# Performance work log

Measured on AMD Instinct MI355X. Metric: run time of the kernel, lower is better.

## Reference

```python
import jax, jax.numpy as jnp
import numpy as np

NEG_SLOPE = 0.2  # PyG GATConv default negative_slope


def setup_inputs() -> dict:
    key = jax.random.key(0)
    k_x, k_e, k_w, k_as, k_ad = jax.random.split(key, 5)
    B, F, N, D, E, L = 2, 16, 5000, 128, 40000, 3
    x = jax.random.normal(k_x, (B, F, N, D), dtype=jnp.float32)
    edge_index = jax.random.randint(k_e, (B, F, 2, E), 0, N, dtype=jnp.int64)
    Ws = jax.random.normal(k_w, (L, D, D), dtype=jnp.float32) / np.float32(np.sqrt(D))
    att_src = jax.random.normal(k_as, (L, D), dtype=jnp.float32) / np.float32(np.sqrt(D))
    att_dst = jax.random.normal(k_ad, (L, D), dtype=jnp.float32) / np.float32(np.sqrt(D))
    bias = jnp.zeros((L, D), dtype=jnp.float32)
    return {"x": x, "edge_index": edge_index, "Ws": Ws,
            "att_src": att_src, "att_dst": att_dst, "bias": bias}


def _gat_layer(h, src, dst, n, W, a_s, a_d, b):
    # h: [n, D] node features; src/dst: [E_tot] edge endpoints (self-loops included)
    h2 = h @ W                                   # [n, D] transformed features
    s = h2 @ a_s                                 # [n] per-node source score
    d = h2 @ a_d                                 # [n] per-node dest score
    e = jax.nn.leaky_relu(s[src] + d[dst], NEG_SLOPE)   # [E_tot] raw attention
    m = jax.lax.stop_gradient(jax.ops.segment_max(e, dst, num_segments=n))
    ex = jnp.exp(e - m[dst])                     # numerically stable softmax per dst
    denom = jax.ops.segment_sum(ex, dst, num_segments=n)
    alpha = ex / denom[dst]                      # [E_tot] normalized attention
    out = jax.ops.segment_sum(alpha[:, None] * h2[src], dst, num_segments=n) + b
    return jax.nn.relu(out)


def reference(x, edge_index, Ws, att_src, att_dst, bias):
    B, F, N, D = x.shape
    n = B * F * N
    h = x.reshape(n, D)
    # faithful to torch: (BF,2,E).view(2,-1) is a raw row-major reshape
    ei = edge_index.reshape(2, -1)
    loop = jnp.arange(n, dtype=ei.dtype)         # PyG GATConv adds self-loops
    src = jnp.concatenate([ei[0], loop])
    dst = jnp.concatenate([ei[1], loop])
    for l in range(Ws.shape[0]):                 # fixed small layer loop
        h = _gat_layer(h, src, dst, n, Ws[l], att_src[l], att_dst[l], bias[l])
    return h.reshape(B, F, N, D)
```

## Files before the change

### kernel.cpp

```cpp
#include <hip/hip_runtime.h>
#include <math.h>

#define NODES_TOTAL 160000
#define NODES_REAL  5000
#define D 128
#define NEG 0.2f
#define KP 136
#define HL (128 * KP)
#define WT_L (2 * HL)

typedef unsigned short ushort_t;
typedef unsigned int uint_t;
typedef __attribute__((ext_vector_type(8))) __bf16 bf16x8;
typedef __attribute__((ext_vector_type(4))) float f32x4;
union BF8 { bf16x8 v; ushort_t u[8]; };

__device__ __forceinline__ void split2(float x, ushort_t& hi, ushort_t& lo) {
    unsigned u = __float_as_uint(x);
    hi = (ushort_t)(u >> 16);
    float hif = __uint_as_float(u & 0xffff0000u);
    lo = (ushort_t)(__float_as_uint(x - hif) >> 16);
}
__device__ __forceinline__ uint_t encmax(float f) {
    uint_t b = __float_as_uint(f);
    return b ^ ((uint_t)((int)b >> 31) | 0x80000000u);
}
__device__ __forceinline__ float decmax(uint_t u) {
    uint_t b = (u & 0x80000000u) ? (u ^ 0x80000000u) : ~u;
    return __uint_as_float(b);
}

__global__ void zero_kernel(int* counts, uint_t* gmaxu) {
    int i = blockIdx.x * blockDim.x + threadIdx.x;
    if (i < NODES_REAL) counts[i] = 0;
    if (i < 3) gmaxu[i] = 0u;
}

__global__ void rank_kernel(const int* __restrict__ ei, int* __restrict__ counts,
                            ushort_t* __restrict__ rank16, int Eh) {
    int e = blockIdx.x * blockDim.x + threadIdx.x;
    if (e < Eh) {
        int d = ei[Eh + e];
        int r = atomicAdd(&counts[d], 1);
        rank16[e] = (ushort_t)r;
    }
}

__global__ void scan_kernel(const int* __restrict__ counts, int* __restrict__ offs) {
    __shared__ int sd[1024];
    int t = threadIdx.x;
    int pre[5]; int sum = 0;
    #pragma unroll
    for (int u = 0; u < 5; ++u) {
        int idx = t * 5 + u;
        int c = (idx < NODES_REAL) ? counts[idx] : 0;
        pre[u] = sum; sum += c;
    }
    sd[t] = sum;
    __syncthreads();
    int run = sum;
    for (int o = 1; o < 1024; o <<= 1) {
        int v = (t >= o) ? sd[t - o] : 0;
        __syncthreads();
        sd[t] += v;
        __syncthreads();
    }
    int excl = sd[t] - run;
    #pragma unroll
    for (int u = 0; u < 5; ++u) {
        int idx = t * 5 + u;
        if (idx < NODES_REAL) offs[idx] = excl + pre[u];
    }
    if (t == 1023) offs[NODES_REAL] = excl + run;
}

__global__ void scatter_det(const int* __restrict__ ei, const int* __restrict__ offs,
                            const ushort_t* __restrict__ rank16, ushort_t* __restrict__ esrc,
                            int Eh) {
    int e = blockIdx.x * blockDim.x + threadIdx.x;
    if (e < Eh) {
        int s = ei[e];
        int d = ei[Eh + e];
        esrc[offs[d] + (int)rank16[e]] = (ushort_t)s;
    }
}

__global__ void wsplit_kernel(const float* __restrict__ Ws, ushort_t* __restrict__ Wt) {
    int l  = blockIdx.x >> 3;
    int n  = (blockIdx.x & 7) * 16 + (threadIdx.x >> 4);
    int k0 = (threadIdx.x & 15) * 8;
    const float* src = Ws + (size_t)l * D * D;
    union { ushort_t u[8]; uint4 v; } hi, lo;
    #pragma unroll
    for (int j = 0; j < 8; ++j) split2(src[(size_t)(k0 + j) * D + n], hi.u[j], lo.u[j]);
    ushort_t* dhi = Wt + (size_t)l * WT_L + n * KP + k0;
    *(uint4*)dhi = hi.v;
    *(uint4*)(dhi + HL) = lo.v;
}

__global__ __launch_bounds__(256)
void mlp3_kernel(const float* __restrict__ x, const ushort_t* __restrict__ Wt,
                 const float* __restrict__ bs, float* __restrict__ out) {
    __shared__ ushort_t Wl[WT_L];
    __shared__ float scr[4][2][16][132];
    int tid = threadIdx.x;
    int w = tid >> 6, lane = tid & 63, q = lane >> 4, m16 = lane & 15;
    int row0 = NODES_REAL + blockIdx.x * 128 + w * 32;

    float4 xa[2][4][2];
    #pragma unroll
    for (int rt = 0; rt < 2; ++rt) {
        int r = row0 + rt * 16 + m16;
        if (r > NODES_TOTAL - 1) r = NODES_TOTAL - 1;
        #pragma unroll
        for (int kc = 0; kc < 4; ++kc) {
            const float* gp = x + (size_t)r * D + kc * 32 + q * 8;
            xa[rt][kc][0] = *(const float4*)gp;
            xa[rt][kc][1] = *(const float4*)(gp + 4);
        }
    }

    f32x4 acc[2][8];
    #pragma unroll
    for (int l = 0; l < 3; ++l) {
        __syncthreads();
        {
            const uint4* gw = (const uint4*)(Wt + (size_t)l * WT_L);
            uint4* lw = (uint4*)Wl;
            #pragma unroll
            for (int r = 0; r < 17; ++r) lw[r * 256 + tid] = gw[r * 256 + tid];
        }
        __syncthreads();

        #pragma unroll
        for (int rt = 0; rt < 2; ++rt)
            #pragma unroll
            for (int ct = 0; ct < 8; ++ct) acc[rt][ct] = (f32x4){0.f, 0.f, 0.f, 0.f};

        #pragma unroll
        for (int kc = 0; kc < 4; ++kc) {
            BF8 ahi[2], alo[2];
            #pragma unroll
            for (int rt = 0; rt < 2; ++rt) {
                float xv[8];
                if (l == 0) {
                    float4 v0 = xa[rt][kc][0], v1 = xa[rt][kc][1];
                    xv[0]=v0.x; xv[1]=v0.y; xv[2]=v0.z; xv[3]=v0.w;
                    xv[4]=v1.x; xv[5]=v1.y; xv[6]=v1.z; xv[7]=v1.w;
                } else {
                    const float* sp = &scr[w][rt][m16][kc * 32 + q * 8];
                    float4 v0 = *(const float4*)sp, v1 = *(const float4*)(sp + 4);
                    xv[0]=v0.x; xv[1]=v0.y; xv[2]=v0.z; xv[3]=v0.w;
                    xv[4]=v1.x; xv[5]=v1.y; xv[6]=v1.z; xv[7]=v1.w;
                }
                #pragma unroll
                for (int j = 0; j < 8; ++j) split2(xv[j], ahi[rt].u[j], alo[rt].u[j]);
            }
            #pragma unroll
            for (int ct = 0; ct < 8; ++ct) {
                const ushort_t* bp = Wl + (ct * 16 + m16) * KP + kc * 32 + q * 8;
                bf16x8 bhi = *(const bf16x8*)bp;
                bf16x8 blo = *(const bf16x8*)(bp + HL);
                #pragma unroll
                for (int rt = 0; rt < 2; ++rt) {
                    acc[rt][ct] = __builtin_amdgcn_mfma_f32_16x16x32_bf16(ahi[rt].v, bhi, acc[rt][ct], 0, 0, 0);
                    acc[rt][ct] = __builtin_amdgcn_mfma_f32_16x16x32_bf16(ahi[rt].v, blo, acc[rt][ct], 0, 0, 0);
                    acc[rt][ct] = __builtin_amdgcn_mfma_f32_16x16x32_bf16(alo[rt].v, bhi, acc[rt][ct], 0, 0, 0);
                }
            }
        }
        float bv[8];
        #pragma unroll
        for (int ct = 0; ct < 8; ++ct) bv[ct] = bs[l * D + ct * 16 + m16];
        #pragma unroll
        for (int rt = 0; rt < 2; ++rt)
            #pragma unroll
            for (int ct = 0; ct < 8; ++ct)
                #pragma unroll
                for (int reg = 0; reg < 4; ++reg)
                    scr[w][rt][q * 4 + reg][ct * 16 + m16] =
                        fmaxf(acc[rt][ct][reg] + bv[ct], 0.f);
    }
    #pragma unroll
    for (int i = 0; i < 16; ++i) {
        int rowl = i * 2 + (lane >> 5);
        int rt = rowl >> 4, r16 = rowl & 15;
        int grow = row0 + rowl;
        float4 v = *(const float4*)&scr[w][rt][r16][(lane & 31) * 4];
        if (grow < NODES_TOTAL)
            *(float4*)&out[(size_t)grow * D + (lane & 31) * 4] = v;
    }
}

__global__ __launch_bounds__(256)
void gsmall_kernel(const float* __restrict__ hin, const ushort_t* __restrict__ Wlg,
                   const float* __restrict__ a_s, const float* __restrict__ a_d,
                   float* __restrict__ h2, float* __restrict__ sv, float* __restrict__ dv,
                   uint_t* __restrict__ gmaxu) {
    __shared__ ushort_t Wl[WT_L];
    int tid = threadIdx.x;
    {
        const uint4* gw = (const uint4*)Wlg;
        uint4* lw = (uint4*)Wl;
        #pragma unroll
        for (int r = 0; r < 17; ++r) lw[r * 256 + tid] = gw[r * 256 + tid];
    }
    int w = tid >> 6, lane = tid & 63, q = lane >> 4, m16 = lane & 15;
    int row0 = blockIdx.x * 128 + w * 32;
    f32x4 acc[2][8];
    #pragma unroll
    for (int rt = 0; rt < 2; ++rt)
        #pragma unroll
        for (int ct = 0; ct < 8; ++ct) acc[rt][ct] = (f32x4){0.f, 0.f, 0.f, 0.f};
    float4 xa[2][4][2];
    #pragma unroll
    for (int rt = 0; rt < 2; ++rt) {
        int r = row0 + rt * 16 + m16;
        if (r > NODES_REAL - 1) r = NODES_REAL - 1;
        #pragma unroll
        for (int kc = 0; kc < 4; ++kc) {
            const float* gp = hin + (size_t)r * D + kc * 32 + q * 8;
            xa[rt][kc][0] = *(const float4*)gp;
            xa[rt][kc][1] = *(const float4*)(gp + 4);
        }
    }
    __syncthreads();
    #pragma unroll
    for (int kc = 0; kc < 4; ++kc) {
        BF8 ahi[2], alo[2];
        #pragma unroll
        for (int rt = 0; rt < 2; ++rt) {
            float4 v0 = xa[rt][kc][0], v1 = xa[rt][kc][1];
            float xv[8] = {v0.x, v0.y, v0.z, v0.w, v1.x, v1.y, v1.z, v1.w};
            #pragma unroll
            for (int j = 0; j < 8; ++j) split2(xv[j], ahi[rt].u[j], alo[rt].u[j]);
        }
        #pragma unroll
        for (int ct = 0; ct < 8; ++ct) {
            const ushort_t* bp = Wl + (ct * 16 + m16) * KP + kc * 32 + q * 8;
            bf16x8 bhi = *(const bf16x8*)bp;
            bf16x8 blo = *(const bf16x8*)(bp + HL);
            #pragma unroll
            for (int rt = 0; rt < 2; ++rt) {
                acc[rt][ct] = __builtin_amdgcn_mfma_f32_16x16x32_bf16(ahi[rt].v, bhi, acc[rt][ct], 0, 0, 0);
                acc[rt][ct] = __builtin_amdgcn_mfma_f32_16x16x32_bf16(ahi[rt].v, blo, acc[rt][ct], 0, 0, 0);
                acc[rt][ct] = __builtin_amdgcn_mfma_f32_16x16x32_bf16(alo[rt].v, bhi, acc[rt][ct], 0, 0, 0);
            }
        }
    }
    #pragma unroll
    for (int rt = 0; rt < 2; ++rt)
        #pragma unroll
        for (int reg = 0; reg < 4; ++reg) {
            int grow = row0 + rt * 16 + q * 4 + reg;
            if (grow < NODES_REAL) {
                #pragma unroll
                for (int ct = 0; ct < 8; ++ct)
                    h2[(size_t)grow * D + ct * 16 + m16] = acc[rt][ct][reg];
            }
        }
    float asv[8], adv[8];
    #pragma unroll
    for (int ct = 0; ct < 8; ++ct) { asv[ct] = a_s[ct * 16 + m16]; adv[ct] = a_d[ct * 16 + m16]; }
    #pragma unroll
    for (int rt = 0; rt < 2; ++rt)
        #pragma unroll
        for (int reg = 0; reg < 4; ++reg) {
            float ps = 0.f, pd = 0.f;
            #pragma unroll
            for (int ct = 0; ct < 8; ++ct) {
                float v = acc[rt][ct][reg];
                ps += v * asv[ct]; pd += v * adv[ct];
            }
            #pragma unroll
            for (int o = 1; o < 16; o <<= 1) { ps += __shfl_xor(ps, o); pd += __shfl_xor(pd, o); }
            int grow = row0 + rt * 16 + q * 4 + reg;
            if (m16 == 0 && grow < NODES_REAL) {
                sv[grow] = ps; dv[grow] = pd;
                atomicMax(gmaxu, encmax(ps));
            }
        }
}

__global__ __launch_bounds__(256)
void agg_kernel(const float* __restrict__ h2, const float* __restrict__ sv,
                const float* __restrict__ dv, const int* __restrict__ offs,
                const ushort_t* __restrict__ esrc, const float* __restrict__ bias,
                float* __restrict__ out, const uint_t* __restrict__ gmaxu) {
    int w = threadIdx.x >> 6, lane = threadIdx.x & 63;
    int i = blockIdx.x * 4 + w;
    int start = offs[i], end = offs[i + 1];
    float d_i = dv[i];
    float gm = decmax(*gmaxu) + d_i;
    float m = gm > 0.f ? gm : NEG * gm;
    float ax = 0.f, ay = 0.f, exs = 0.f;
    for (int base = start; base < end; base += 64) {
        int cnt = min(64, end - base);
        int srci = (lane < cnt) ? (int)esrc[base + lane] : 0;
        float sc = sv[srci] + d_i;
        sc = sc > 0.f ? sc : NEG * sc;
        float ex = (lane < cnt) ? __expf(sc - m) : 0.f;
        exs += ex;
        if (cnt == 64) {
            #pragma unroll 4
            for (int j = 0; j < 64; ++j) {
                int   src = __shfl(srci, j);
                float e   = __shfl(ex, j);
                float2 hv = *(const float2*)&h2[(size_t)src * D + 2 * lane];
                ax += e * hv.x; ay += e * hv.y;
            }
        } else {
            for (int j = 0; j < cnt; ++j) {
                int   src = __shfl(srci, j);
                float e   = __shfl(ex, j);
                float2 hv = *(const float2*)&h2[(size_t)src * D + 2 * lane];
                ax += e * hv.x; ay += e * hv.y;
            }
        }
    }
    float scf = sv[i] + d_i; scf = scf > 0.f ? scf : NEG * scf;
    float exf = __expf(scf - m);
    float2 hv = *(const float2*)&h2[(size_t)i * D + 2 * lane];
    ax += exf * hv.x; ay += exf * hv.y;
    #pragma unroll
    for (int o = 1; o < 64; o <<= 1) exs += __shfl_xor(exs, o);
    float rd = 1.f / (exs + exf);
    float2 b2 = *(const float2*)&bias[2 * lane];
    float2 o2 = make_float2(fmaxf(ax * rd + b2.x, 0.f), fmaxf(ay * rd + b2.y, 0.f));
    *(float2*)&out[(size_t)i * D + 2 * lane] = o2;
}

extern "C" void kernel_launch(void* const* d_in, const int* in_sizes, int n_in,
                              void* d_out, int out_size, void* d_ws, size_t ws_size,
                              hipStream_t stream) {
    const float* x   = (const float*)d_in[0];
    const int*   ei  = (const int*)d_in[1];
    const float* Ws  = (const float*)d_in[2];
    const float* as_ = (const float*)d_in[3];
    const float* ad_ = (const float*)d_in[4];
    const float* bs  = (const float*)d_in[5];
    float* out = (float*)d_out;
    int Eh = in_sizes[1] / 2;

    char* ws = (char*)d_ws;
    float*    h2     = (float*)ws;
    float*    bufS   = (float*)(ws + 2560000);
    float*    sv     = (float*)(ws + 5120000);
    float*    dv     = (float*)(ws + 5140000);
    int*      counts = (int*)  (ws + 5160000);
    int*      offs   = (int*)  (ws + 5180000);
    ushort_t* rank16 = (ushort_t*)(ws + 5200016);
    ushort_t* esrc   = (ushort_t*)(ws + 7760016);
    ushort_t* Wt     = (ushort_t*)(ws + 10320016);
    uint_t*   gmaxu  = (uint_t*)(ws + 10528912);

    zero_kernel<<<(NODES_REAL + 255) / 256, 256, 0, stream>>>(counts, gmaxu);
    rank_kernel<<<(Eh + 255) / 256, 256, 0, stream>>>(ei, counts, rank16, Eh);
    scan_kernel<<<1, 1024, 0, stream>>>(counts, offs);
    scatter_det<<<(Eh + 255) / 256, 256, 0, stream>>>(ei, offs, rank16, esrc, Eh);
    wsplit_kernel<<<24, 256, 0, stream>>>(Ws, Wt);

    mlp3_kernel<<<(NODES_TOTAL - NODES_REAL + 127) / 128, 256, 0, stream>>>(x, Wt, bs, out);

    for (int l = 0; l < 3; ++l) {
        const float* hin = (l == 0) ? x : bufS;
        float* hout = (l == 2) ? out : bufS;
        gsmall_kernel<<<(NODES_REAL + 127) / 128, 256, 0, stream>>>(
            hin, Wt + (size_t)l * WT_L, as_ + l * D, ad_ + l * D, h2, sv, dv, gmaxu + l);
        agg_kernel<<<(NODES_REAL + 3) / 4, 256, 0, stream>>>(
            h2, sv, dv, offs, esrc, bs + l * D, hout, gmaxu + l);
    }
}
```

Measured before the change: 517.6 us.

## Read MLP weights directly from global memory and split agg accumulation into two chains

The isolated-node MLP kernel no longer stages each layer's split bf16 weights into LDS. It reads them from a new unpadded global copy, so the staging copy and a barrier go away and LDS use drops to allow two blocks per CU. The aggregation loop now processes two neighbours per iteration with separate accumulators to expose more memory-level parallelism. In exchange, weight reads now depend on L1/L2 cache hits instead of LDS.

```diff
diff --git a/kernel.cpp b/kernel.cpp
--- a/kernel.cpp
+++ b/kernel.cpp
@@ -8,6 +8,9 @@
 #define KP 136
 #define HL (128 * KP)
 #define WT_L (2 * HL)
+#define KP2 128
+#define HL2 (128 * KP2)
+#define WT2_L (2 * HL2)
 
 typedef unsigned short ushort_t;
 typedef unsigned int uint_t;
@@ -85,7 +88,8 @@
     }
 }
 
-__global__ void wsplit_kernel(const float* __restrict__ Ws, ushort_t* __restrict__ Wt) {
+__global__ void wsplit_kernel(const float* __restrict__ Ws, ushort_t* __restrict__ Wt,
+                              ushort_t* __restrict__ Wu) {
     int l  = blockIdx.x >> 3;
     int n  = (blockIdx.x & 7) * 16 + (threadIdx.x >> 4);
     int k0 = (threadIdx.x & 15) * 8;
@@ -96,12 +100,14 @@
     ushort_t* dhi = Wt + (size_t)l * WT_L + n * KP + k0;
     *(uint4*)dhi = hi.v;
     *(uint4*)(dhi + HL) = lo.v;
-}
-
-__global__ __launch_bounds__(256)
-void mlp3_kernel(const float* __restrict__ x, const ushort_t* __restrict__ Wt,
+    ushort_t* dhi2 = Wu + (size_t)l * WT2_L + n * KP2 + k0;
+    *(uint4*)dhi2 = hi.v;
+    *(uint4*)(dhi2 + HL2) = lo.v;
+}
+
+__global__ __launch_bounds__(256, 2)
+void mlp3_kernel(const float* __restrict__ x, const ushort_t* __restrict__ Wu,
                  const float* __restrict__ bs, float* __restrict__ out) {
-    __shared__ ushort_t Wl[WT_L];
     __shared__ float scr[4][2][16][132];
     int tid = threadIdx.x;
     int w = tid >> 6, lane = tid & 63, q = lane >> 4, m16 = lane & 15;
@@ -123,14 +129,8 @@
     f32x4 acc[2][8];
     #pragma unroll
     for (int l = 0; l < 3; ++l) {
-        __syncthreads();
-        {
-            const uint4* gw = (const uint4*)(Wt + (size_t)l * WT_L);
-            uint4* lw = (uint4*)Wl;
-            #pragma unroll
-            for (int r = 0; r < 17; ++r) lw[r * 256 + tid] = gw[r * 256 + tid];
-        }
-        __syncthreads();
+        if (l > 0) __syncthreads();
+        const ushort_t* Wb = Wu + (size_t)l * WT2_L + m16 * KP2 + q * 8;
 
         #pragma unroll
         for (int rt = 0; rt < 2; ++rt)
@@ -158,9 +158,9 @@
             }
             #pragma unroll
             for (int ct = 0; ct < 8; ++ct) {
-                const ushort_t* bp = Wl + (ct * 16 + m16) * KP + kc * 32 + q * 8;
+                const ushort_t* bp = Wb + ct * 16 * KP2 + kc * 32;
                 bf16x8 bhi = *(const bf16x8*)bp;
-                bf16x8 blo = *(const bf16x8*)(bp + HL);
+                bf16x8 blo = *(const bf16x8*)(bp + HL2);
                 #pragma unroll
                 for (int rt = 0; rt < 2; ++rt) {
                     acc[rt][ct] = __builtin_amdgcn_mfma_f32_16x16x32_bf16(ahi[rt].v, bhi, acc[rt][ct], 0, 0, 0);
@@ -293,7 +293,7 @@
     float d_i = dv[i];
     float gm = decmax(*gmaxu) + d_i;
     float m = gm > 0.f ? gm : NEG * gm;
-    float ax = 0.f, ay = 0.f, exs = 0.f;
+    float ax = 0.f, ay = 0.f, ax1 = 0.f, ay1 = 0.f, exs = 0.f;
     for (int base = start; base < end; base += 64) {
         int cnt = min(64, end - base);
         int srci = (lane < cnt) ? (int)esrc[base + lane] : 0;
@@ -303,11 +303,13 @@
         exs += ex;
         if (cnt == 64) {
             #pragma unroll 4
-            for (int j = 0; j < 64; ++j) {
-                int   src = __shfl(srci, j);
-                float e   = __shfl(ex, j);
-                float2 hv = *(const float2*)&h2[(size_t)src * D + 2 * lane];
-                ax += e * hv.x; ay += e * hv.y;
+            for (int j = 0; j < 64; j += 2) {
+                int   s0 = __shfl(srci, j),     s1 = __shfl(srci, j + 1);
+                float e0 = __shfl(ex, j),       e1 = __shfl(ex, j + 1);
+                float2 h0 = *(const float2*)&h2[(size_t)s0 * D + 2 * lane];
+                float2 h1 = *(const float2*)&h2[(size_t)s1 * D + 2 * lane];
+                ax  += e0 * h0.x; ay  += e0 * h0.y;
+                ax1 += e1 * h1.x; ay1 += e1 * h1.y;
             }
         } else {
             for (int j = 0; j < cnt; ++j) {
@@ -318,6 +320,7 @@
             }
         }
     }
+    ax += ax1; ay += ay1;
     float scf = sv[i] + d_i; scf = scf > 0.f ? scf : NEG * scf;
     float exf = __expf(scf - m);
     float2 hv = *(const float2*)&h2[(size_t)i * D + 2 * lane];
@@ -353,14 +356,15 @@
     ushort_t* esrc   = (ushort_t*)(ws + 7760016);
     ushort_t* Wt     = (ushort_t*)(ws + 10320016);
     uint_t*   gmaxu  = (uint_t*)(ws + 10528912);
+    ushort_t* Wu     = (ushort_t*)(ws + 10528928);
 
     zero_kernel<<<(NODES_REAL + 255) / 256, 256, 0, stream>>>(counts, gmaxu);
     rank_kernel<<<(Eh + 255) / 256, 256, 0, stream>>>(ei, counts, rank16, Eh);
     scan_kernel<<<1, 1024, 0, stream>>>(counts, offs);
     scatter_det<<<(Eh + 255) / 256, 256, 0, stream>>>(ei, offs, rank16, esrc, Eh);
-    wsplit_kernel<<<24, 256, 0, stream>>>(Ws, Wt);
-
-    mlp3_kernel<<<(NODES_TOTAL - NODES_REAL + 127) / 128, 256, 0, stream>>>(x, Wt, bs, out);
+    wsplit_kernel<<<24, 256, 0, stream>>>(Ws, Wt, Wu);
+
+    mlp3_kernel<<<(NODES_TOTAL - NODES_REAL + 127) / 128, 256, 0, stream>>>(x, Wu, bs, out);
 
     for (int l = 0; l < 3; ++l) {
         const float* hin = (l == 0) ? x : bufS;
```

Result: slower. 591.3 us (+14.2%).

## Split mlp3 output columns across wave pairs with 512-thread blocks; dual accumulators in agg

Applied to the files above, without the earlier changes.

The dense MLP kernel for the isolated nodes now uses 512 threads per block. Pairs of waves share a 32-row tile, and each wave computes half of the 128 output columns, which halves per-wave accumulators and doubles the waves available to hide latency. Because waves now share the scratch tile, inputs for later layers are preloaded from shared memory before a barrier, and the final write is preceded by one. In the aggregation kernel, the 64-edge inner loop is unrolled by two with separate accumulators to increase memory-level parallelism on the gathered rows.

```diff
diff --git a/kernel.cpp b/kernel.cpp
--- a/kernel.cpp
+++ b/kernel.cpp
@@ -98,14 +98,15 @@
     *(uint4*)(dhi + HL) = lo.v;
 }
 
-__global__ __launch_bounds__(256)
+__global__ __launch_bounds__(512)
 void mlp3_kernel(const float* __restrict__ x, const ushort_t* __restrict__ Wt,
                  const float* __restrict__ bs, float* __restrict__ out) {
     __shared__ ushort_t Wl[WT_L];
     __shared__ float scr[4][2][16][132];
     int tid = threadIdx.x;
     int w = tid >> 6, lane = tid & 63, q = lane >> 4, m16 = lane & 15;
-    int row0 = NODES_REAL + blockIdx.x * 128 + w * 32;
+    int p = w >> 1, h = w & 1;
+    int row0 = NODES_REAL + blockIdx.x * 128 + p * 32;
 
     float4 xa[2][4][2];
     #pragma unroll
@@ -120,7 +121,7 @@
         }
     }
 
-    f32x4 acc[2][8];
+    f32x4 acc[2][4];
     #pragma unroll
     for (int l = 0; l < 3; ++l) {
         __syncthreads();
@@ -128,37 +129,40 @@
             const uint4* gw = (const uint4*)(Wt + (size_t)l * WT_L);
             uint4* lw = (uint4*)Wl;
             #pragma unroll
-            for (int r = 0; r < 17; ++r) lw[r * 256 + tid] = gw[r * 256 + tid];
+            for (int r = 0; r < 8; ++r) lw[r * 512 + tid] = gw[r * 512 + tid];
+            if (tid < 256) lw[4096 + tid] = gw[4096 + tid];
+        }
+        if (l > 0) {
+            #pragma unroll
+            for (int rt = 0; rt < 2; ++rt)
+                #pragma unroll
+                for (int kc = 0; kc < 4; ++kc) {
+                    const float* sp = &scr[p][rt][m16][kc * 32 + q * 8];
+                    xa[rt][kc][0] = *(const float4*)sp;
+                    xa[rt][kc][1] = *(const float4*)(sp + 4);
+                }
         }
         __syncthreads();
 
         #pragma unroll
         for (int rt = 0; rt < 2; ++rt)
             #pragma unroll
-            for (int ct = 0; ct < 8; ++ct) acc[rt][ct] = (f32x4){0.f, 0.f, 0.f, 0.f};
+            for (int ct = 0; ct < 4; ++ct) acc[rt][ct] = (f32x4){0.f, 0.f, 0.f, 0.f};
 
         #pragma unroll
         for (int kc = 0; kc < 4; ++kc) {
             BF8 ahi[2], alo[2];
             #pragma unroll
             for (int rt = 0; rt < 2; ++rt) {
-                float xv[8];
-                if (l == 0) {
-                    float4 v0 = xa[rt][kc][0], v1 = xa[rt][kc][1];
-                    xv[0]=v0.x; xv[1]=v0.y; xv[2]=v0.z; xv[3]=v0.w;
-                    xv[4]=v1.x; xv[5]=v1.y; xv[6]=v1.z; xv[7]=v1.w;
-                } else {
-                    const float* sp = &scr[w][rt][m16][kc * 32 + q * 8];
-                    float4 v0 = *(const float4*)sp, v1 = *(const float4*)(sp + 4);
-                    xv[0]=v0.x; xv[1]=v0.y; xv[2]=v0.z; xv[3]=v0.w;
-                    xv[4]=v1.x; xv[5]=v1.y; xv[6]=v1.z; xv[7]=v1.w;
-                }
+                float4 v0 = xa[rt][kc][0], v1 = xa[rt][kc][1];
+                float xv[8] = {v0.x, v0.y, v0.z, v0.w, v1.x, v1.y, v1.z, v1.w};
                 #pragma unroll
                 for (int j = 0; j < 8; ++j) split2(xv[j], ahi[rt].u[j], alo[rt].u[j]);
             }
             #pragma unroll
-            for (int ct = 0; ct < 8; ++ct) {
-                const ushort_t* bp = Wl + (ct * 16 + m16) * KP + kc * 32 + q * 8;
+            for (int ct = 0; ct < 4; ++ct) {
+                int ctg = h * 4 + ct;
+                const ushort_t* bp = Wl + (ctg * 16 + m16) * KP + kc * 32 + q * 8;
                 bf16x8 bhi = *(const bf16x8*)bp;
                 bf16x8 blo = *(const bf16x8*)(bp + HL);
                 #pragma unroll
@@ -169,24 +173,24 @@
                 }
             }
         }
-        float bv[8];
-        #pragma unroll
-        for (int ct = 0; ct < 8; ++ct) bv[ct] = bs[l * D + ct * 16 + m16];
+        float bv[4];
+        #pragma unroll
+        for (int ct = 0; ct < 4; ++ct) bv[ct] = bs[l * D + (h * 4 + ct) * 16 + m16];
         #pragma unroll
         for (int rt = 0; rt < 2; ++rt)
             #pragma unroll
-            for (int ct = 0; ct < 8; ++ct)
+            for (int ct = 0; ct < 4; ++ct)
                 #pragma unroll
                 for (int reg = 0; reg < 4; ++reg)
-                    scr[w][rt][q * 4 + reg][ct * 16 + m16] =
+                    scr[p][rt][q * 4 + reg][(h * 4 + ct) * 16 + m16] =
                         fmaxf(acc[rt][ct][reg] + bv[ct], 0.f);
     }
-    #pragma unroll
-    for (int i = 0; i < 16; ++i) {
+    __syncthreads();
+    #pragma unroll
+    for (int i = 0; i < 8; ++i) {
         int rowl = i * 2 + (lane >> 5);
-        int rt = rowl >> 4, r16 = rowl & 15;
-        int grow = row0 + rowl;
-        float4 v = *(const float4*)&scr[w][rt][r16][(lane & 31) * 4];
+        int grow = row0 + h * 16 + rowl;
+        float4 v = *(const float4*)&scr[p][h][rowl][(lane & 31) * 4];
         if (grow < NODES_TOTAL)
             *(float4*)&out[(size_t)grow * D + (lane & 31) * 4] = v;
     }
@@ -293,7 +297,7 @@
     float d_i = dv[i];
     float gm = decmax(*gmaxu) + d_i;
     float m = gm > 0.f ? gm : NEG * gm;
-    float ax = 0.f, ay = 0.f, exs = 0.f;
+    float ax = 0.f, ay = 0.f, ax1 = 0.f, ay1 = 0.f, exs = 0.f;
     for (int base = start; base < end; base += 64) {
         int cnt = min(64, end - base);
         int srci = (lane < cnt) ? (int)esrc[base + lane] : 0;
@@ -303,11 +307,13 @@
         exs += ex;
         if (cnt == 64) {
             #pragma unroll 4
-            for (int j = 0; j < 64; ++j) {
-                int   src = __shfl(srci, j);
-                float e   = __shfl(ex, j);
-                float2 hv = *(const float2*)&h2[(size_t)src * D + 2 * lane];
-                ax += e * hv.x; ay += e * hv.y;
+            for (int j = 0; j < 64; j += 2) {
+                int   s0 = __shfl(srci, j),     s1 = __shfl(srci, j + 1);
+                float e0 = __shfl(ex, j),       e1 = __shfl(ex, j + 1);
+                float2 h0 = *(const float2*)&h2[(size_t)s0 * D + 2 * lane];
+                float2 h1 = *(const float2*)&h2[(size_t)s1 * D + 2 * lane];
+                ax  += e0 * h0.x; ay  += e0 * h0.y;
+                ax1 += e1 * h1.x; ay1 += e1 * h1.y;
             }
         } else {
             for (int j = 0; j < cnt; ++j) {
@@ -318,6 +324,7 @@
             }
         }
     }
+    ax += ax1; ay += ay1;
     float scf = sv[i] + d_i; scf = scf > 0.f ? scf : NEG * scf;
     float exf = __expf(scf - m);
     float2 hv = *(const float2*)&h2[(size_t)i * D + 2 * lane];
@@ -360,7 +367,7 @@
     scatter_det<<<(Eh + 255) / 256, 256, 0, stream>>>(ei, offs, rank16, esrc, Eh);
     wsplit_kernel<<<24, 256, 0, stream>>>(Ws, Wt);
 
-    mlp3_kernel<<<(NODES_TOTAL - NODES_REAL + 127) / 128, 256, 0, stream>>>(x, Wt, bs, out);
+    mlp3_kernel<<<(NODES_TOTAL - NODES_REAL + 127) / 128, 512, 0, stream>>>(x, Wt, bs, out);
 
     for (int l = 0; l < 3; ++l) {
         const float* hin = (l == 0) ? x : bufS;
```

Measured after the change: 517.2 us. No clear change (-0.1%).
